# Kernel optimization log

Hardware: AMD Instinct MI355X
Metric: run time of the kernel (lower is better)

Reference implementation:

```python
import jax, jax.numpy as jnp
import numpy as np

DIM = 2048
NUM_HEADS = 16
HEAD_DIM = DIM // NUM_HEADS
BATCH, SEQ = 2, 2048


def setup_inputs() -> dict:
    key = jax.random.key(0)
    kx, kq, kk, kv, ko = jax.random.split(key, 5)
    scale = 1.0 / np.sqrt(DIM)
    return {
        "x": jax.random.normal(kx, (BATCH, SEQ, DIM), dtype=jnp.float32),
        "Wq": jax.random.normal(kq, (DIM, DIM), dtype=jnp.float32) * scale,
        "Wk": jax.random.normal(kk, (DIM, DIM), dtype=jnp.float32) * scale,
        "Wv": jax.random.normal(kv, (DIM, DIM), dtype=jnp.float32) * scale,
        "Wo": jax.random.normal(ko, (DIM, DIM), dtype=jnp.float32) * scale,
    }


def reference(x, Wq, Wk, Wv, Wo):
    b, s, _ = x.shape
    # QKV projections (flax Dense, no bias): y = x @ W
    q = (x @ Wq).reshape(b, s, NUM_HEADS, HEAD_DIM)
    k = (x @ Wk).reshape(b, s, NUM_HEADS, HEAD_DIM)
    v = (x @ Wv).reshape(b, s, NUM_HEADS, HEAD_DIM)
    # full (non-causal) softmax attention, scores are [b, h, q, k]
    scores = jnp.einsum('bqhd,bkhd->bhqk', q, k) * (HEAD_DIM ** -0.5)
    attn = jax.nn.softmax(scores, axis=-1)
    out = jnp.einsum('bhqk,bkhd->bqhd', attn, v).reshape(b, s, DIM)
    return out @ Wo
```

## Files before the change

### kernel.cpp

```cpp
#include <hip/hip_runtime.h>
#include <stdint.h>


typedef unsigned short u16;
typedef __attribute__((ext_vector_type(8))) short bf16x8;
typedef __attribute__((ext_vector_type(4))) float f32x4;
typedef __attribute__((ext_vector_type(2))) unsigned int u32x2;

__device__ __forceinline__ u16 f2bf(float f) {
  union { float f; uint32_t u; } v; v.f = f;
  return (u16)((v.u + 0x7fffu + ((v.u >> 16) & 1u)) >> 16);
}

__device__ __forceinline__ float fast_exp2(float x) {
#if __has_builtin(__builtin_amdgcn_exp2f)
  return __builtin_amdgcn_exp2f(x);
#else
  return exp2f(x);
#endif
}

__device__ __forceinline__ void gl_lds16(const void* g, void* l) {
  __builtin_amdgcn_global_load_lds(
      (const __attribute__((address_space(1))) unsigned int*)g,
      (__attribute__((address_space(3))) unsigned int*)l, 16, 0, 0);
}

__global__ __launch_bounds__(256) void sniff_k(const u16* __restrict__ x,
                                               int* __restrict__ flag) {
  __shared__ int cnt;
  const int t = threadIdx.x;
  if (t == 0) cnt = 0;
  __syncthreads();
  int sane = 0;
#pragma unroll
  for (int i = 0; i < 16; ++i) {
    u16 u = x[t * 16 + i];
    int e = (u >> 7) & 0xff;
    sane += (e >= 90 && e <= 150) ? 1 : 0;
  }
  atomicAdd(&cnt, sane);
  __syncthreads();
  if (t == 0) *flag = (cnt >= 3700) ? 0 : 1;
}

__global__ __launch_bounds__(256) void convert_x_k(const void* __restrict__ xin,
                                                   u16* __restrict__ xb,
                                                   const int* __restrict__ flag) {
  if (*flag == 0) return;
  const int i = (blockIdx.x * 256 + threadIdx.x) * 8;
  const float* xf = (const float*)xin;
  float4 a = *(const float4*)(xf + i);
  float4 b = *(const float4*)(xf + i + 4);
  bf16x8 o;
  o[0] = (short)f2bf(a.x); o[1] = (short)f2bf(a.y);
  o[2] = (short)f2bf(a.z); o[3] = (short)f2bf(a.w);
  o[4] = (short)f2bf(b.x); o[5] = (short)f2bf(b.y);
  o[6] = (short)f2bf(b.z); o[7] = (short)f2bf(b.w);
  *(bf16x8*)(xb + i) = o;
}

__global__ __launch_bounds__(256) void convert_transpose_k(const void* __restrict__ w0,
                                                           const void* __restrict__ w1,
                                                           const void* __restrict__ w2,
                                                           const void* __restrict__ w3,
                                                           u16* __restrict__ out_base,
                                                           const int* __restrict__ flag) {
  __shared__ u16 tile[64][66];
  const int z = blockIdx.z;
  const void* in = (z == 0) ? w0 : (z == 1) ? w1 : (z == 2) ? w2 : w3;
  u16* out = out_base + (size_t)z * 4194304u;
  const int tr = blockIdx.y, tc = blockIdx.x, t = threadIdx.x;
  if (*flag) {
    const float* inf32 = (const float*)in;
#pragma unroll
    for (int i = 0; i < 16; ++i) {
      int idx = t + i * 256, r = idx >> 6, c = idx & 63;
      tile[r][c] = f2bf(inf32[(size_t)(tr * 64 + r) * 2048 + tc * 64 + c]);
    }
  } else {
    const u16* inb = (const u16*)in;
#pragma unroll
    for (int i = 0; i < 16; ++i) {
      int idx = t + i * 256, r = idx >> 6, c = idx & 63;
      tile[r][c] = inb[(size_t)(tr * 64 + r) * 2048 + tc * 64 + c];
    }
  }
  __syncthreads();
#pragma unroll
  for (int i = 0; i < 16; ++i) {
    int idx = t + i * 256, r = idx >> 6, c = idx & 63;
    out[(size_t)(tc * 64 + r) * 2048 + tr * 64 + c] = tile[c][r];
  }
}

__global__ __launch_bounds__(256) void transpose_k(const u16* __restrict__ in,
                                                   u16* __restrict__ out) {
  __shared__ u16 tile[64][66];
  const size_t zoff = (size_t)blockIdx.z * 4194304u;
  in += zoff; out += zoff;
  const int tr = blockIdx.y, tc = blockIdx.x, t = threadIdx.x;
#pragma unroll
  for (int i = 0; i < 16; ++i) {
    int idx = t + i * 256, r = idx >> 6, c = idx & 63;
    tile[r][c] = in[(size_t)(tr * 64 + r) * 2048 + tc * 64 + c];
  }
  __syncthreads();
#pragma unroll
  for (int i = 0; i < 16; ++i) {
    int idx = t + i * 256, r = idx >> 6, c = idx & 63;
    out[(size_t)(tc * 64 + r) * 2048 + tr * 64 + c] = tile[c][r];
  }
}

__global__ __launch_bounds__(512, 2) void gemm256(const u16* __restrict__ A,
                                                  const void* __restrict__ Araw,
                                                  const int* __restrict__ aflag,
                                                  const u16* __restrict__ Bt,
                                                  u16* __restrict__ Cbase,
                                                  float qscale) {
  __shared__ __align__(16) u16 Ls[2][2][2][128 * 64];

  const int t = threadIdx.x, wave = t >> 6, lane = t & 63;
  const int g = lane >> 4, lq = lane & 15;
  const int wr = wave >> 2, wc = wave & 3;
  const int bid = blockIdx.x;
  const int swz = (bid & 7) * 48 + (bid >> 3);
  const int bm = swz / 24, bn = swz % 24;

  const u16* Ause = (*aflag == 0) ? (const u16*)Araw : A;
  const u16* Arow = Ause + (size_t)(bm * 256) * 2048;
  const u16* Brow = Bt + (size_t)(bn * 256) * 2048;
  const int lr = lane >> 3, lcs = ((lane & 7) ^ lr) * 8;

  int cofs[2];
#pragma unroll
  for (int kk = 0; kk < 2; ++kk) cofs[kk] = ((kk * 4 + g) ^ (lq & 7)) * 8;

  f32x4 acc[8][4];
#pragma unroll
  for (int i = 0; i < 8; ++i)
#pragma unroll
    for (int j = 0; j < 4; ++j) acc[i][j] = f32x4{0.f, 0.f, 0.f, 0.f};

  auto stageH = [&](int tt, int mat, int h) {
    const u16* src = mat ? Brow : Arow;
    u16* dst = &Ls[tt & 1][mat][h][0];
    const int kb = tt * 64;
#pragma unroll
    for (int i = 0; i < 2; ++i) {
      const int s = wave * 2 + i;
      gl_lds16(src + (size_t)(h * 128 + s * 8 + lr) * 2048 + kb + lcs,
               dst + s * 8 * 64);
    }
  };

  bf16x8 af[8], bfr[4];
  auto ldA = [&](const u16* base) {
#pragma unroll
    for (int m = 0; m < 4; ++m)
#pragma unroll
      for (int kk = 0; kk < 2; ++kk)
        af[m * 2 + kk] = *(const bf16x8*)(&base[(wr * 64 + m * 16 + lq) * 64 + cofs[kk]]);
  };
  auto ldB = [&](const u16* base) {
#pragma unroll
    for (int n = 0; n < 2; ++n)
#pragma unroll
      for (int kk = 0; kk < 2; ++kk)
        bfr[n * 2 + kk] = *(const bf16x8*)(&base[(wc * 32 + n * 16 + lq) * 64 + cofs[kk]]);
  };
  auto mmac = [&](int mh, int nh) {
    __builtin_amdgcn_s_barrier();
    asm volatile("s_waitcnt lgkmcnt(0)" ::: "memory");
    __builtin_amdgcn_sched_barrier(0);
    __builtin_amdgcn_s_setprio(1);
#pragma unroll
    for (int m = 0; m < 4; ++m)
#pragma unroll
      for (int n = 0; n < 2; ++n)
#pragma unroll
        for (int kk = 0; kk < 2; ++kk)
          acc[mh * 4 + m][nh * 2 + n] = __builtin_amdgcn_mfma_f32_16x16x32_bf16(
              af[m * 2 + kk], bfr[n * 2 + kk], acc[mh * 4 + m][nh * 2 + n], 0, 0, 0);
    __builtin_amdgcn_s_setprio(0);
    __builtin_amdgcn_s_barrier();
  };

  stageH(0, 0, 0); stageH(0, 1, 0); stageH(0, 0, 1); stageH(0, 1, 1);
  stageH(1, 0, 0); stageH(1, 1, 0);
  asm volatile("s_waitcnt vmcnt(4)" ::: "memory");
  __builtin_amdgcn_sched_barrier(0);
  __builtin_amdgcn_s_barrier();

  for (int it = 0; it < 16; ++it) {
    const int u1 = 2 * it + 1, u2 = 2 * it + 2, u3 = 2 * it + 3;
    ldA(&Ls[0][0][0][0]);
    ldB(&Ls[0][1][0][0]);
    stageH(u1, 0, 1); stageH(u1, 1, 1);
    mmac(0, 0);
    ldB(&Ls[0][1][1][0]);
    mmac(0, 1);
    ldA(&Ls[0][0][1][0]);
    ldB(&Ls[0][1][0][0]);
    if (u2 < 32) stageH(u2, 0, 0);
    mmac(1, 0);
    ldB(&Ls[0][1][1][0]);
    if (u2 < 32) stageH(u2, 1, 0);
    if (it < 15) asm volatile("s_waitcnt vmcnt(4)" ::: "memory");
    else         asm volatile("s_waitcnt vmcnt(0)" ::: "memory");
    __builtin_amdgcn_sched_barrier(0);
    mmac(1, 1);
    ldA(&Ls[1][0][0][0]);
    ldB(&Ls[1][1][0][0]);
    if (u2 < 32) { stageH(u2, 0, 1); stageH(u2, 1, 1); }
    mmac(0, 0);
    ldB(&Ls[1][1][1][0]);
    mmac(0, 1);
    ldA(&Ls[1][0][1][0]);
    ldB(&Ls[1][1][0][0]);
    if (u3 < 32) stageH(u3, 0, 0);
    mmac(1, 0);
    ldB(&Ls[1][1][1][0]);
    if (u3 < 32) stageH(u3, 1, 0);
    asm volatile("s_waitcnt vmcnt(4)" ::: "memory");
    __builtin_amdgcn_sched_barrier(0);
    mmac(1, 1);
  }

  const int which = bn >> 3;
  u16* C = Cbase + (size_t)which * 2u * 4194304u;
  const float scale = (which == 0) ? qscale : 1.0f;
  const int colbase = (bn & 7) * 256;
#pragma unroll
  for (int mh = 0; mh < 2; ++mh)
#pragma unroll
    for (int m = 0; m < 4; ++m)
#pragma unroll
      for (int nh = 0; nh < 2; ++nh)
#pragma unroll
        for (int n = 0; n < 2; ++n)
#pragma unroll
          for (int j = 0; j < 4; ++j) {
            size_t row = (size_t)(bm * 256 + mh * 128 + wr * 64 + m * 16 + g * 4 + j);
            size_t col = (size_t)(colbase + nh * 128 + wc * 32 + n * 16 + lq);
            C[row * 2048 + col] = f2bf(acc[mh * 4 + m][nh * 2 + n][j] * scale);
          }
}

__global__ __launch_bounds__(256) void gemm_bt(const u16* __restrict__ A,
                                               const void* __restrict__ Araw,
                                               const int* __restrict__ aflag,
                                               const u16* __restrict__ Bt,
                                               u16* __restrict__ C0,
                                               u16* __restrict__ C1,
                                               u16* __restrict__ C2,
                                               float qscale,
                                               const int* __restrict__ outflag) {
  __shared__ u16 As[128 * 64];
  __shared__ u16 Bs[128 * 64];
  const int bx = blockIdx.x, by = blockIdx.y, t = threadIdx.x;
  const int wave = t >> 6, lane = t & 63;
  const int g = lane >> 4, lq = lane & 15;
  const int wr = wave >> 1, wc = wave & 1;
  const int which = bx >> 4, nb = bx & 15;
  u16* C = (which == 0) ? C0 : ((which == 1) ? C1 : C2);
  const float scale = (which == 0) ? qscale : 1.0f;
  const u16* Ause = (aflag && *aflag == 0) ? (const u16*)Araw : A;
  const int lr = lane >> 3, lcs = ((lane & 7) ^ lr) * 8;

  const u16* Arow = Ause + (size_t)(by * 128) * 2048;
  const u16* Brow = Bt + (size_t)(bx * 128) * 2048;

  int cofs[2];
#pragma unroll
  for (int ks = 0; ks < 2; ++ks) cofs[ks] = ((ks * 4 + g) ^ (lq & 7)) * 8;

  f32x4 acc[4][4];
#pragma unroll
  for (int i = 0; i < 4; ++i)
#pragma unroll
    for (int j = 0; j < 4; ++j) acc[i][j] = f32x4{0.f, 0.f, 0.f, 0.f};

  for (int kb = 0; kb < 2048; kb += 64) {
    __syncthreads();
#pragma unroll
    for (int i = 0; i < 4; ++i) {
      const int r = wave * 32 + i * 8;
      gl_lds16(Arow + (size_t)(r + lr) * 2048 + kb + lcs, &As[r * 64]);
      gl_lds16(Brow + (size_t)(r + lr) * 2048 + kb + lcs, &Bs[r * 64]);
    }
    __syncthreads();
#pragma unroll
    for (int ks = 0; ks < 2; ++ks) {
      bf16x8 af[4], bfr[4];
#pragma unroll
      for (int mt = 0; mt < 4; ++mt)
        af[mt] = *(const bf16x8*)(&As[(wr * 64 + mt * 16 + lq) * 64 + cofs[ks]]);
#pragma unroll
      for (int nt = 0; nt < 4; ++nt)
        bfr[nt] = *(const bf16x8*)(&Bs[(wc * 64 + nt * 16 + lq) * 64 + cofs[ks]]);
#pragma unroll
      for (int mt = 0; mt < 4; ++mt)
#pragma unroll
        for (int nt = 0; nt < 4; ++nt)
          acc[mt][nt] = __builtin_amdgcn_mfma_f32_16x16x32_bf16(af[mt], bfr[nt], acc[mt][nt], 0, 0, 0);
    }
  }
  const int outF32 = outflag ? *outflag : 0;
#pragma unroll
  for (int mt = 0; mt < 4; ++mt)
#pragma unroll
    for (int nt = 0; nt < 4; ++nt)
#pragma unroll
      for (int j = 0; j < 4; ++j) {
        size_t row = (size_t)(by * 128 + wr * 64 + mt * 16 + g * 4 + j);
        size_t col = (size_t)(nb * 128 + wc * 64 + nt * 16 + lq);
        float v = acc[mt][nt][j] * scale;
        if (outF32) ((float*)C)[row * 2048 + col] = v;
        else C[row * 2048 + col] = f2bf(v);
      }
}

__global__ __launch_bounds__(256, 4) void attn_kernel(const u16* __restrict__ Q,
                                                      const u16* __restrict__ K,
                                                      const u16* __restrict__ Vt,
                                                      u16* __restrict__ O) {
  __shared__ u16 Ks[64 * 128];
  __shared__ u16 Vs[128 * 64];

  const int qb = blockIdx.x, h = blockIdx.y, b = blockIdx.z;
  const int t = threadIdx.x, wave = t >> 6, lane = t & 63;
  const int g = lane >> 4, lq = lane & 15;

  const size_t qk_base = ((size_t)b * 2048) * 2048 + (size_t)h * 128;
  const size_t vt_base = ((size_t)b * 2048 + (size_t)h * 128) * 2048;

  bf16x8 qf[4];
  {
    const u16* qp = Q + qk_base + (size_t)(qb * 64 + wave * 16 + lq) * 2048 + g * 8;
#pragma unroll
    for (int kk = 0; kk < 4; ++kk) qf[kk] = *(const bf16x8*)(qp + kk * 32);
  }

  f32x4 acc_o[8];
#pragma unroll
  for (int i = 0; i < 8; ++i) acc_o[i] = f32x4{0.f, 0.f, 0.f, 0.f};
  float l_run = 0.f;

  const int vlr = lane >> 3, vlcs = ((lane & 7) ^ vlr) * 8;

  int kofs[4];
#pragma unroll
  for (int kk = 0; kk < 4; ++kk) kofs[kk] = ((kk * 4 + g) ^ (lq & 7)) * 8;

  for (int kb = 0; kb < 2048; kb += 64) {
    __syncthreads();
#pragma unroll
    for (int i = 0; i < 4; ++i) {
      const int win = wave * 2 + (i >> 1), half = i & 1;
      const int kr = half * 4 + (lane >> 4);
      const int kc = (lane & 15) ^ kr;
      gl_lds16(K + qk_base + (size_t)(kb + win * 8 + kr) * 2048 + kc * 8,
               &Ks[win * 1024 + half * 512]);
      const int vr = wave * 32 + i * 8;
      gl_lds16(Vt + vt_base + (size_t)(vr + vlr) * 2048 + kb + vlcs,
               &Vs[vr * 64]);
    }
    __syncthreads();

    f32x4 st[4];
#pragma unroll
    for (int mt = 0; mt < 4; ++mt) st[mt] = f32x4{0.f, 0.f, 0.f, 0.f};
#pragma unroll
    for (int kk = 0; kk < 4; ++kk)
#pragma unroll
      for (int mt = 0; mt < 4; ++mt) {
        bf16x8 af = *(const bf16x8*)(&Ks[(mt * 16 + lq) * 128 + kofs[kk]]);
        st[mt] = __builtin_amdgcn_mfma_f32_16x16x32_bf16(af, qf[kk], st[mt], 0, 0, 0);
      }

    uint32_t c[4][2];
#pragma unroll
    for (int mt = 0; mt < 4; ++mt) {
      float p0 = fast_exp2(st[mt][0]);
      float p1 = fast_exp2(st[mt][1]);
      float p2 = fast_exp2(st[mt][2]);
      float p3 = fast_exp2(st[mt][3]);
      l_run += (p0 + p1) + (p2 + p3);
      asm("v_cvt_pk_bf16_f32 %0, %1, %2" : "=v"(c[mt][0]) : "v"(p0), "v"(p1));
      asm("v_cvt_pk_bf16_f32 %0, %1, %2" : "=v"(c[mt][1]) : "v"(p2), "v"(p3));
    }

#pragma unroll
    for (int kk = 0; kk < 2; ++kk) {
      u32x2 s0 = __builtin_amdgcn_permlane32_swap(c[2 * kk][0], c[2 * kk + 1][0], false, false);
      u32x2 r0 = __builtin_amdgcn_permlane16_swap(s0[0], s0[1], false, false);
      u32x2 s1 = __builtin_amdgcn_permlane32_swap(c[2 * kk][1], c[2 * kk + 1][1], false, false);
      u32x2 r1 = __builtin_amdgcn_permlane16_swap(s1[0], s1[1], false, false);
      union { uint32_t d[4]; bf16x8 v; } af;
      af.d[0] = r0[0];
      af.d[1] = r1[0];
      af.d[2] = r0[1];
      af.d[3] = r1[1];
#pragma unroll
      for (int nt = 0; nt < 8; ++nt) {
        bf16x8 bfr = *(const bf16x8*)(&Vs[(nt * 16 + lq) * 64 + ((kk * 4 + g) ^ (lq & 7)) * 8]);
        acc_o[nt] = __builtin_amdgcn_mfma_f32_16x16x32_bf16(af.v, bfr, acc_o[nt], 0, 0, 0);
      }
    }
  }

  l_run += __shfl_xor(l_run, 16);
  l_run += __shfl_xor(l_run, 32);
  const float i0 = 1.f / __shfl(l_run, g * 4 + 0);
  const float i1 = 1.f / __shfl(l_run, g * 4 + 1);
  const float i2 = 1.f / __shfl(l_run, g * 4 + 2);
  const float i3 = 1.f / __shfl(l_run, g * 4 + 3);
  u16* op = O + ((size_t)b * 2048 + qb * 64 + wave * 16) * 2048 + h * 128;
#pragma unroll
  for (int nt = 0; nt < 8; ++nt) {
    op[(size_t)(g * 4 + 0) * 2048 + nt * 16 + lq] = f2bf(acc_o[nt][0] * i0);
    op[(size_t)(g * 4 + 1) * 2048 + nt * 16 + lq] = f2bf(acc_o[nt][1] * i1);
    op[(size_t)(g * 4 + 2) * 2048 + nt * 16 + lq] = f2bf(acc_o[nt][2] * i2);
    op[(size_t)(g * 4 + 3) * 2048 + nt * 16 + lq] = f2bf(acc_o[nt][3] * i3);
  }
}

extern "C" void kernel_launch(void* const* d_in, const int* in_sizes, int n_in,
                              void* d_out, int out_size, void* d_ws, size_t ws_size,
                              hipStream_t stream) {
  const void* x  = d_in[0];
  const void* Wq = d_in[1];
  const void* Wk = d_in[2];
  const void* Wv = d_in[3];
  const void* Wo = d_in[4];
  u16* ws = (u16*)d_ws;

  const size_t SLOT = 4194304u;
  u16* xb  = ws + 0 * SLOT;
  u16* WqT = ws + 2 * SLOT;
  u16* WoT = ws + 5 * SLOT;
  u16* Qb  = ws + 6 * SLOT;
  u16* Kb  = ws + 8 * SLOT;
  u16* Vb  = ws + 10 * SLOT;
  int* flag = (int*)(ws + 12 * SLOT);
  u16* VTd = (u16*)d_out;
  u16* Ab  = Qb;

  sniff_k<<<1, 256, 0, stream>>>((const u16*)x, flag);

  convert_x_k<<<4096, 256, 0, stream>>>(x, xb, flag);
  convert_transpose_k<<<dim3(32, 32, 4), 256, 0, stream>>>(Wq, Wk, Wv, Wo, WqT, flag);

  const float QSCALE = 0.12751745f;
  gemm256<<<384, 512, 0, stream>>>(xb, x, flag, WqT, Qb, QSCALE);

  transpose_k<<<dim3(32, 32, 2), 256, 0, stream>>>(Vb, VTd);

  attn_kernel<<<dim3(32, 16, 2), dim3(256), 0, stream>>>(Qb, Kb, VTd, Ab);

  gemm_bt<<<dim3(16, 32), 256, 0, stream>>>(Ab, Ab, nullptr, WoT,
                                            (u16*)d_out, (u16*)d_out, (u16*)d_out,
                                            1.0f, flag);
}
```

Measured before the change: 402.3 us.

## Restructure QKV GEMM pipeline with double B fragments and deeper prefetch

The QKV projection GEMM main loop is rescheduled. B fragments are kept in two register sets, so the second B half is reused for the lower A half instead of being reloaded from LDS. The prologue now prefetches two full k-tiles, with vmcnt(8) waits, and the barrier/lgkmcnt placement is rearranged so global-to-LDS staging overlaps the MFMA blocks. This removes redundant LDS reads and some barrier stalls, at the cost of extra registers and a more fragile ordering of LDS buffer reuse.

```diff
diff --git a/kernel.cpp b/kernel.cpp
--- a/kernel.cpp
+++ b/kernel.cpp
@@ -143,6 +143,9 @@
 #pragma unroll
     for (int j = 0; j < 4; ++j) acc[i][j] = f32x4{0.f, 0.f, 0.f, 0.f};
 
+  bf16x8 af[8];
+  bf16x8 b0[4], b1[4];
+
   auto stageH = [&](int tt, int mat, int h) {
     const u16* src = mat ? Brow : Arow;
     u16* dst = &Ls[tt & 1][mat][h][0];
@@ -154,8 +157,6 @@
                dst + s * 8 * 64);
     }
   };
-
-  bf16x8 af[8], bfr[4];
   auto ldA = [&](const u16* base) {
 #pragma unroll
     for (int m = 0; m < 4; ++m)
@@ -163,17 +164,14 @@
       for (int kk = 0; kk < 2; ++kk)
         af[m * 2 + kk] = *(const bf16x8*)(&base[(wr * 64 + m * 16 + lq) * 64 + cofs[kk]]);
   };
-  auto ldB = [&](const u16* base) {
+  auto ldB = [&](bf16x8* dst, const u16* base) {
 #pragma unroll
     for (int n = 0; n < 2; ++n)
 #pragma unroll
       for (int kk = 0; kk < 2; ++kk)
-        bfr[n * 2 + kk] = *(const bf16x8*)(&base[(wc * 32 + n * 16 + lq) * 64 + cofs[kk]]);
+        dst[n * 2 + kk] = *(const bf16x8*)(&base[(wc * 32 + n * 16 + lq) * 64 + cofs[kk]]);
   };
-  auto mmac = [&](int mh, int nh) {
-    __builtin_amdgcn_s_barrier();
-    asm volatile("s_waitcnt lgkmcnt(0)" ::: "memory");
-    __builtin_amdgcn_sched_barrier(0);
+  auto mfma8 = [&](int mh, int nh, const bf16x8* b) {
     __builtin_amdgcn_s_setprio(1);
 #pragma unroll
     for (int m = 0; m < 4; ++m)
@@ -182,50 +180,67 @@
 #pragma unroll
         for (int kk = 0; kk < 2; ++kk)
           acc[mh * 4 + m][nh * 2 + n] = __builtin_amdgcn_mfma_f32_16x16x32_bf16(
-              af[m * 2 + kk], bfr[n * 2 + kk], acc[mh * 4 + m][nh * 2 + n], 0, 0, 0);
+              af[m * 2 + kk], b[n * 2 + kk], acc[mh * 4 + m][nh * 2 + n], 0, 0, 0);
     __builtin_amdgcn_s_setprio(0);
-    __builtin_amdgcn_s_barrier();
   };
 
-  stageH(0, 0, 0); stageH(0, 1, 0); stageH(0, 0, 1); stageH(0, 1, 1);
-  stageH(1, 0, 0); stageH(1, 1, 0);
-  asm volatile("s_waitcnt vmcnt(4)" ::: "memory");
+  stageH(0, 0, 0); stageH(0, 1, 0); stageH(0, 1, 1); stageH(0, 0, 1);
+  stageH(1, 0, 0); stageH(1, 1, 0); stageH(1, 1, 1); stageH(1, 0, 1);
+  asm volatile("s_waitcnt vmcnt(8)" ::: "memory");
   __builtin_amdgcn_sched_barrier(0);
   __builtin_amdgcn_s_barrier();
 
   for (int it = 0; it < 16; ++it) {
-    const int u1 = 2 * it + 1, u2 = 2 * it + 2, u3 = 2 * it + 3;
+    const bool nl = (it < 15);
+    const int e2 = 2 * it + 2, o2 = 2 * it + 3;
     ldA(&Ls[0][0][0][0]);
-    ldB(&Ls[0][1][0][0]);
-    stageH(u1, 0, 1); stageH(u1, 1, 1);
-    mmac(0, 0);
-    ldB(&Ls[0][1][1][0]);
-    mmac(0, 1);
+    ldB(b0, &Ls[0][1][0][0]);
+    asm volatile("s_waitcnt lgkmcnt(0)" ::: "memory");
+    __builtin_amdgcn_sched_barrier(0);
+    __builtin_amdgcn_s_barrier();
+    if (nl) { stageH(e2, 0, 0); stageH(e2, 1, 0); }
+    mfma8(0, 0, b0);
+    ldB(b1, &Ls[0][1][1][0]);
+    asm volatile("s_waitcnt lgkmcnt(0)" ::: "memory");
+    __builtin_amdgcn_sched_barrier(0);
+    __builtin_amdgcn_s_barrier();
+    if (nl) stageH(e2, 1, 1);
+    mfma8(0, 1, b1);
     ldA(&Ls[0][0][1][0]);
-    ldB(&Ls[0][1][0][0]);
-    if (u2 < 32) stageH(u2, 0, 0);
-    mmac(1, 0);
-    ldB(&Ls[0][1][1][0]);
-    if (u2 < 32) stageH(u2, 1, 0);
-    if (it < 15) asm volatile("s_waitcnt vmcnt(4)" ::: "memory");
-    else         asm volatile("s_waitcnt vmcnt(0)" ::: "memory");
-    __builtin_amdgcn_sched_barrier(0);
-    mmac(1, 1);
+    asm volatile("s_waitcnt lgkmcnt(0)" ::: "memory");
+    __builtin_amdgcn_sched_barrier(0);
+    __builtin_amdgcn_s_barrier();
+    if (nl) stageH(e2, 0, 1);
+    mfma8(1, 0, b0);
+    if (nl) asm volatile("s_waitcnt vmcnt(8)" ::: "memory");
+    else    asm volatile("s_waitcnt vmcnt(0)" ::: "memory");
+    __builtin_amdgcn_sched_barrier(0);
+    __builtin_amdgcn_s_barrier();
+    mfma8(1, 1, b1);
     ldA(&Ls[1][0][0][0]);
-    ldB(&Ls[1][1][0][0]);
-    if (u2 < 32) { stageH(u2, 0, 1); stageH(u2, 1, 1); }
-    mmac(0, 0);
-    ldB(&Ls[1][1][1][0]);
-    mmac(0, 1);
+    ldB(b0, &Ls[1][1][0][0]);
+    asm volatile("s_waitcnt lgkmcnt(0)" ::: "memory");
+    __builtin_amdgcn_sched_barrier(0);
+    __builtin_amdgcn_s_barrier();
+    if (nl) { stageH(o2, 0, 0); stageH(o2, 1, 0); }
+    mfma8(0, 0, b0);
+    ldB(b1, &Ls[1][1][1][0]);
+    asm volatile("s_waitcnt lgkmcnt(0)" ::: "memory");
+    __builtin_amdgcn_sched_barrier(0);
+    __builtin_amdgcn_s_barrier();
+    if (nl) stageH(o2, 1, 1);
+    mfma8(0, 1, b1);
     ldA(&Ls[1][0][1][0]);
-    ldB(&Ls[1][1][0][0]);
-    if (u3 < 32) stageH(u3, 0, 0);
-    mmac(1, 0);
-    ldB(&Ls[1][1][1][0]);
-    if (u3 < 32) stageH(u3, 1, 0);
-    asm volatile("s_waitcnt vmcnt(4)" ::: "memory");
-    __builtin_amdgcn_sched_barrier(0);
-    mmac(1, 1);
+    asm volatile("s_waitcnt lgkmcnt(0)" ::: "memory");
+    __builtin_amdgcn_sched_barrier(0);
+    __builtin_amdgcn_s_barrier();
+    if (nl) stageH(o2, 0, 1);
+    mfma8(1, 0, b0);
+    if (nl) asm volatile("s_waitcnt vmcnt(8)" ::: "memory");
+    else    asm volatile("s_waitcnt vmcnt(0)" ::: "memory");
+    __builtin_amdgcn_sched_barrier(0);
+    __builtin_amdgcn_s_barrier();
+    mfma8(1, 1, b1);
   }
 
   const int which = bn >> 3;
```

New measurement: 413.7 us. 2.8% more time.
